# Performance work log

Hardware: AMD Instinct MI355X
Metric: run time of the kernel (lower is better)

## Reference

```python
import jax, jax.numpy as jnp
import numpy as np

B, H, T, D = 2, 16, 2048, 64


def setup_inputs() -> dict:
    key = jax.random.key(0)
    kq, kk, kv, kvm, khm = jax.random.split(key, 5)
    q = jax.random.normal(kq, (B, H, T, D), dtype=jnp.float32)
    k = jax.random.normal(kk, (B, H, D, T), dtype=jnp.float32)  # pre-transposed, matmul(q, k) -> [B,H,T,T]
    v = jax.random.normal(kv, (B, H, T, D), dtype=jnp.float32)
    f = jnp.asarray(float(np.sqrt(D)), dtype=jnp.float32)  # scale divisor
    vmask = (jax.random.uniform(kvm, (B, T)) < 0.9).astype(jnp.float32)
    hmask = (jax.random.uniform(khm, (B, T)) < 0.9).astype(jnp.float32)
    return {"q": q, "k": k, "v": v, "f": f, "vmask": vmask, "hmask": hmask}


def reference(q, k, v, f, vmask, hmask):
    # scores = q @ k / f  -> [B,H,T,T]
    scores = jnp.matmul(q, k) / f
    # padding mask: vmask indexes columns (key positions), hmask indexes rows (query positions)
    pad = vmask[:, None, None, :] * hmask[:, None, :, None]  # [B,1,T,T], broadcasts over H
    s = scores * pad
    s = jnp.where(s == 0, jnp.asarray(1e-10, s.dtype), s)  # masked_fill(new_scores == 0, 1e-10)
    # causal mask: -inf strictly above diagonal
    t = s.shape[-1]
    causal = jnp.triu(jnp.full((t, t), -jnp.inf, dtype=s.dtype), k=1)
    s = s + causal
    return jnp.matmul(jax.nn.softmax(s, axis=-1), v)  # [B,H,T,D]
```

## Files before the change

### kernel.cpp

```cpp
#include <hip/hip_runtime.h>
#include <hip/hip_bf16.h>

#define B_ 2
#define H_ 16
#define T_ 2048
#define D_ 64
#define BH (B_*H_)

typedef __attribute__((ext_vector_type(8))) short bf16x8;
typedef __attribute__((ext_vector_type(16))) float f32x16;
typedef __attribute__((ext_vector_type(4))) unsigned int u32x4;
typedef unsigned int u32;

typedef __attribute__((address_space(3))) void lds_void;
typedef __attribute__((address_space(1))) const void gbl_void;

__device__ __forceinline__ ushort f2bu(float x){
    __hip_bfloat16 h = __float2bfloat16(x);
    return __builtin_bit_cast(ushort, h);
}
__device__ __forceinline__ u32 cvtpk(float a, float b){
    u32 r; asm("v_cvt_pk_bf16_f32 %0, %1, %2" : "=v"(r) : "v"(a), "v"(b)); return r;
}
__device__ __forceinline__ float xhalf_max(float x){
    float a = x, b = x;
    asm("" : "+v"(b));
    asm("v_permlane32_swap_b32 %0, %1" : "+v"(a), "+v"(b));
    return fmaxf(a, b);
}
__device__ __forceinline__ float xhalf_sum(float x){
    float a = x, b = x;
    asm("" : "+v"(b));
    asm("v_permlane32_swap_b32 %0, %1" : "+v"(a), "+v"(b));
    return a + b;
}

__global__ __launch_bounds__(256) void prep(
    const float* __restrict__ k, const float* __restrict__ v,
    const float* __restrict__ vm,
    ushort* __restrict__ KT, ushort* __restrict__ VT)
{
    __shared__ ushort tl[64][65];
    const int bh = blockIdx.x;
    const bool isK = (blockIdx.y < 32);
    const int ty = isK ? blockIdx.y : (blockIdx.y - 32);
    const int i0 = isK ? 0 : ty*64;
    const int j0 = isK ? ty*64 : 0;
    const int M = isK ? D_ : T_;
    const int N = isK ? T_ : D_;
    const float* s = (isK ? k : v) + (size_t)bh*M*N;
    ushort*      d = (isK ? KT : VT) + (size_t)bh*M*N;
    const int tid = threadIdx.x;
    const int rr = tid>>4, c4 = (tid&15)*4;
    #pragma unroll
    for (int p=0;p<4;++p){
        int a = p*16+rr;
        float4 x = *reinterpret_cast<const float4*>(&s[(size_t)(i0+a)*N + j0 + c4]);
        tl[c4+0][a]=f2bu(x.x); tl[c4+1][a]=f2bu(x.y);
        tl[c4+2][a]=f2bu(x.z); tl[c4+3][a]=f2bu(x.w);
    }
    __syncthreads();
    #pragma unroll
    for (int p=0;p<4;++p){
        int bb = p*16+rr;
        ushort4 u;
        u.x=tl[bb][c4]; u.y=tl[bb][c4+1]; u.z=tl[bb][c4+2]; u.w=tl[bb][c4+3];
        if (isK && vm[(size_t)(bh>>4)*T_ + j0 + bb] == 0.f) { u.x=0;u.y=0;u.z=0;u.w=0; }
        *reinterpret_cast<ushort4*>(&d[(size_t)(j0+bb)*M + i0 + c4]) = u;
    }
}

__global__ __launch_bounds__(64, 2) void attn_fwd(
    const float* __restrict__ q, const float* __restrict__ fp,
    const float* __restrict__ hmask,
    const ushort* __restrict__ KT,
    const ushort* __restrict__ VT,
    float* __restrict__ out)
{
    __shared__ __align__(16) ushort sbuf[2][8192];

    const int bid = blockIdx.x;
    const int bh = bid & (BH-1);
    const int qw = 63 - (bid >> 5);
    const int i0 = qw*32;
    const int lane = threadIdx.x & 63;
    const int col = lane & 31;
    const int hi  = lane >> 5;

    const ushort* KTb = KT + (size_t)bh*T_*D_;
    const ushort* VTb = VT + (size_t)bh*T_*D_;

    const float hmv = hmask[(size_t)(bh>>4)*T_ + i0 + col];
    const float sscale = 1.4426950408889634f / fp[0];
    const float qs = (hmv != 0.f) ? sscale : 0.f;
    const float NINF = -__builtin_inff();

    const float* qp = q + (size_t)bh*T_*D_ + (size_t)(i0+col)*D_ + hi*8;
    bf16x8 qf[4];
    #pragma unroll
    for (int dc=0; dc<4; ++dc){
        float4 x0 = *reinterpret_cast<const float4*>(qp + dc*16);
        float4 x1 = *reinterpret_cast<const float4*>(qp + dc*16 + 4);
        u32x4 dw;
        dw[0] = cvtpk(x0.x*qs, x0.y*qs);
        dw[1] = cvtpk(x0.z*qs, x0.w*qs);
        dw[2] = cvtpk(x1.x*qs, x1.y*qs);
        dw[3] = cvtpk(x1.z*qs, x1.w*qs);
        qf[dc] = __builtin_bit_cast(bf16x8, dw);
    }

    float m_run = NINF, l_run = 0.f;
    f32x16 o0, o1;
    #pragma unroll
    for (int r=0;r<16;++r){ o0[r]=0.f; o1[r]=0.f; }

    const unsigned uoff = (unsigned)(lane*16);
    const unsigned swz = ((unsigned)(col&7)) << 4;

    auto stage = [&](int b, int t){
        char* ldsK = (char*)&sbuf[b][0];
        char* ldsV = (char*)&sbuf[b][4096];
        const char* kbase = (const char*)KTb + (size_t)t*8192;
        #pragma unroll
        for (int i=0;i<8;++i){
            const unsigned u = i*1024u + uoff;
            const unsigned su = u ^ (((u>>7)&7u)<<4);
            __builtin_amdgcn_global_load_lds(
                (gbl_void*)(kbase + su),
                (lds_void*)(ldsK + i*1024), 16, 0, 0);
        }
        #pragma unroll
        for (int i=0;i<8;++i){
            const unsigned u = i*1024u + uoff;
            const unsigned dR = u>>7;
            const unsigned inr = (u&127u) ^ ((dR&7u)<<4);
            const char* src = (const char*)VTb + (size_t)dR*(T_*2) + (size_t)t*128 + inr;
            __builtin_amdgcn_global_load_lds(
                (gbl_void*)src,
                (lds_void*)(ldsV + i*1024), 16, 0, 0);
        }
    };

    const int n = (qw >> 1) + 1;
    int buf = 0;
    stage(0, 0);
    asm volatile("s_waitcnt vmcnt(0)" ::: "memory");

    for (int t=0; t<n; ++t){
        const int j0 = t*64;
        if (t+1 < n) stage(buf^1, t+1);

        const char* sKb = (const char*)&sbuf[buf][0];
        bf16x8 kf[8];
        #pragma unroll
        for (int kt=0;kt<2;++kt)
            #pragma unroll
            for (int dc=0;dc<4;++dc)
                kf[kt*4+dc] = *reinterpret_cast<const bf16x8*>(
                    sKb + (((unsigned)(kt*4096 + dc*32 + col*128 + hi*16)) ^ swz));

        f32x16 s0, s1;
        #pragma unroll
        for (int r=0;r<16;++r){ s0[r]=0.f; s1[r]=0.f; }
        #pragma unroll
        for (int dc=0;dc<4;++dc){
            s0 = __builtin_amdgcn_mfma_f32_32x32x16_bf16(kf[dc],   qf[dc], s0, 0,0,0);
            s1 = __builtin_amdgcn_mfma_f32_32x32x16_bf16(kf[4+dc], qf[dc], s1, 0,0,0);
        }

        const char* sVb = (const char*)&sbuf[buf][4096];
        bf16x8 vf[8];
        #pragma unroll
        for (int f=0;f<8;++f)
            vf[f] = *reinterpret_cast<const bf16x8*>(
                sVb + (((unsigned)((f>>2)*4096 + (f&3)*32 + col*128 + hi*16)) ^ swz));

        if (j0 + 63 > i0) {
            const int th0 = i0 + col - j0 - 4*hi;
            const int th1 = th0 - 32;
            #pragma unroll
            for (int r=0;r<16;++r){
                const int basr = (r&3) + 8*(r>>2);
                s0[r] = (basr <= th0) ? s0[r] : NINF;
                s1[r] = (basr <= th1) ? s1[r] : NINF;
            }
        }

        float tm[8];
        #pragma unroll
        for (int i=0;i<8;++i)
            tm[i] = fmaxf(fmaxf(s0[2*i], s0[2*i+1]), fmaxf(s1[2*i], s1[2*i+1]));
        #pragma unroll
        for (int st=4; st>=1; st>>=1)
            #pragma unroll
            for (int i=0;i<st;++i) tm[i] = fmaxf(tm[i], tm[i+st]);
        const float mt = xhalf_max(tm[0]);

        if (__any(!(mt <= m_run + 8.0f))) {
            const float mn = fmaxf(m_run, mt);
            const float fac = __builtin_amdgcn_exp2f(m_run - mn);
            m_run = mn;
            l_run *= fac;
            #pragma unroll
            for (int r=0;r<16;++r){ o0[r]*=fac; o1[r]*=fac; }
        }

        float tsum[8];
        #pragma unroll
        for (int i=0;i<8;++i){
            float p00 = __builtin_amdgcn_exp2f(s0[2*i]   - m_run);
            float p01 = __builtin_amdgcn_exp2f(s0[2*i+1] - m_run);
            float p10 = __builtin_amdgcn_exp2f(s1[2*i]   - m_run);
            float p11 = __builtin_amdgcn_exp2f(s1[2*i+1] - m_run);
            s0[2*i]=p00; s0[2*i+1]=p01; s1[2*i]=p10; s1[2*i+1]=p11;
            tsum[i] = (p00+p01) + (p10+p11);
        }
        #pragma unroll
        for (int st=4; st>=1; st>>=1)
            #pragma unroll
            for (int i=0;i<st;++i) tsum[i] += tsum[i+st];
        l_run += xhalf_sum(tsum[0]);

        bf16x8 pb[4];
        #pragma unroll
        for (int c2=0;c2<4;++c2){
            const f32x16& ps = (c2<2) ? s0 : s1;
            const int rb = (c2&1)*8;
            u32 a0 = cvtpk(ps[rb+0], ps[rb+1]);
            u32 a1 = cvtpk(ps[rb+2], ps[rb+3]);
            u32 a2 = cvtpk(ps[rb+4], ps[rb+5]);
            u32 a3 = cvtpk(ps[rb+6], ps[rb+7]);
            asm("v_permlane32_swap_b32 %0, %1" : "+v"(a0), "+v"(a2));
            asm("v_permlane32_swap_b32 %0, %1" : "+v"(a1), "+v"(a3));
            u32x4 dw; dw[0]=a0; dw[1]=a1; dw[2]=a2; dw[3]=a3;
            pb[c2] = __builtin_bit_cast(bf16x8, dw);
        }

        #pragma unroll
        for (int c2=0;c2<4;++c2){
            o0 = __builtin_amdgcn_mfma_f32_32x32x16_bf16(vf[c2],   pb[c2], o0, 0,0,0);
            o1 = __builtin_amdgcn_mfma_f32_32x32x16_bf16(vf[4+c2], pb[c2], o1, 0,0,0);
        }

        asm volatile("s_waitcnt vmcnt(0)" ::: "memory");
        buf ^= 1;
    }

    const float rinv = 1.0f / l_run;
    float* op = out + (size_t)bh*T_*D_ + (size_t)(i0+col)*D_;
    #pragma unroll
    for (int q4=0;q4<4;++q4){
        float4 a = {o0[4*q4]*rinv, o0[4*q4+1]*rinv, o0[4*q4+2]*rinv, o0[4*q4+3]*rinv};
        *reinterpret_cast<float4*>(op + 8*q4 + 4*hi) = a;
        float4 b = {o1[4*q4]*rinv, o1[4*q4+1]*rinv, o1[4*q4+2]*rinv, o1[4*q4+3]*rinv};
        *reinterpret_cast<float4*>(op + 32 + 8*q4 + 4*hi) = b;
    }
}

extern "C" void kernel_launch(void* const* d_in, const int* in_sizes, int n_in,
                              void* d_out, int out_size, void* d_ws, size_t ws_size,
                              hipStream_t stream) {
    const float* q  = (const float*)d_in[0];
    const float* k  = (const float*)d_in[1];
    const float* v  = (const float*)d_in[2];
    const float* f  = (const float*)d_in[3];
    const float* vm = (const float*)d_in[4];
    const float* hm = (const float*)d_in[5];
    float* out = (float*)d_out;

    const size_t slab = (size_t)BH * T_ * D_;
    ushort* KT = (ushort*)d_ws;
    ushort* VT = KT + slab;

    hipLaunchKernelGGL(prep, dim3(BH, 64), dim3(256), 0, stream, k, v, vm, KT, VT);

    dim3 grid(2048);
    dim3 block(64);
    hipLaunchKernelGGL(attn_fwd, grid, block, 0, stream, q, f, hm, KT, VT, out);
}
```

Baseline: 57.25 us.

## Process two 32-row query tiles per wave to reuse staged K/V tiles

```diff
diff --git a/kernel.cpp b/kernel.cpp
--- a/kernel.cpp
+++ b/kernel.cpp
@@ -81,8 +81,9 @@
 
     const int bid = blockIdx.x;
     const int bh = bid & (BH-1);
-    const int qw = 63 - (bid >> 5);
-    const int i0 = qw*32;
+    const int idx = bid >> 5;
+    const int qw = (bid < 512) ? (31 - idx) : (idx - 16);
+    const int i0 = qw*64;
     const int lane = threadIdx.x & 63;
     const int col = lane & 31;
     const int hi  = lane >> 5;
@@ -90,29 +91,42 @@
     const ushort* KTb = KT + (size_t)bh*T_*D_;
     const ushort* VTb = VT + (size_t)bh*T_*D_;
 
-    const float hmv = hmask[(size_t)(bh>>4)*T_ + i0 + col];
     const float sscale = 1.4426950408889634f / fp[0];
-    const float qs = (hmv != 0.f) ? sscale : 0.f;
+    const float hmA = hmask[(size_t)(bh>>4)*T_ + i0 + col];
+    const float hmB = hmask[(size_t)(bh>>4)*T_ + i0 + 32 + col];
+    const float qsA = (hmA != 0.f) ? sscale : 0.f;
+    const float qsB = (hmB != 0.f) ? sscale : 0.f;
     const float NINF = -__builtin_inff();
 
-    const float* qp = q + (size_t)bh*T_*D_ + (size_t)(i0+col)*D_ + hi*8;
-    bf16x8 qf[4];
+    bf16x8 qfA[4], qfB[4];
+    {
+        const float* qpA = q + (size_t)bh*T_*D_ + (size_t)(i0+col)*D_ + hi*8;
+        const float* qpB = qpA + 32*D_;
+        #pragma unroll
+        for (int dc=0; dc<4; ++dc){
+            float4 x0 = *reinterpret_cast<const float4*>(qpA + dc*16);
+            float4 x1 = *reinterpret_cast<const float4*>(qpA + dc*16 + 4);
+            u32x4 dw;
+            dw[0] = cvtpk(x0.x*qsA, x0.y*qsA);
+            dw[1] = cvtpk(x0.z*qsA, x0.w*qsA);
+            dw[2] = cvtpk(x1.x*qsA, x1.y*qsA);
+            dw[3] = cvtpk(x1.z*qsA, x1.w*qsA);
+            qfA[dc] = __builtin_bit_cast(bf16x8, dw);
+            float4 y0 = *reinterpret_cast<const float4*>(qpB + dc*16);
+            float4 y1 = *reinterpret_cast<const float4*>(qpB + dc*16 + 4);
+            u32x4 ew;
+            ew[0] = cvtpk(y0.x*qsB, y0.y*qsB);
+            ew[1] = cvtpk(y0.z*qsB, y0.w*qsB);
+            ew[2] = cvtpk(y1.x*qsB, y1.y*qsB);
+            ew[3] = cvtpk(y1.z*qsB, y1.w*qsB);
+            qfB[dc] = __builtin_bit_cast(bf16x8, ew);
+        }
+    }
+
+    float mA = 0.f, lA = 0.f, mB = 0.f, lB = 0.f;
+    f32x16 oA0, oA1, oB0, oB1;
     #pragma unroll
-    for (int dc=0; dc<4; ++dc){
-        float4 x0 = *reinterpret_cast<const float4*>(qp + dc*16);
-        float4 x1 = *reinterpret_cast<const float4*>(qp + dc*16 + 4);
-        u32x4 dw;
-        dw[0] = cvtpk(x0.x*qs, x0.y*qs);
-        dw[1] = cvtpk(x0.z*qs, x0.w*qs);
-        dw[2] = cvtpk(x1.x*qs, x1.y*qs);
-        dw[3] = cvtpk(x1.z*qs, x1.w*qs);
-        qf[dc] = __builtin_bit_cast(bf16x8, dw);
-    }
-
-    float m_run = NINF, l_run = 0.f;
-    f32x16 o0, o1;
-    #pragma unroll
-    for (int r=0;r<16;++r){ o0[r]=0.f; o1[r]=0.f; }
+    for (int r=0;r<16;++r){ oA0[r]=0.f; oA1[r]=0.f; oB0[r]=0.f; oB1[r]=0.f; }
 
     const unsigned uoff = (unsigned)(lane*16);
     const unsigned swz = ((unsigned)(col&7)) << 4;
@@ -141,7 +155,7 @@
         }
     };
 
-    const int n = (qw >> 1) + 1;
+    const int n = qw + 1;
     int buf = 0;
     stage(0, 0);
     asm volatile("s_waitcnt vmcnt(0)" ::: "memory");
@@ -159,13 +173,15 @@
                 kf[kt*4+dc] = *reinterpret_cast<const bf16x8*>(
                     sKb + (((unsigned)(kt*4096 + dc*32 + col*128 + hi*16)) ^ swz));
 
-        f32x16 s0, s1;
-        #pragma unroll
-        for (int r=0;r<16;++r){ s0[r]=0.f; s1[r]=0.f; }
+        f32x16 sA0, sA1, sB0, sB1;
+        #pragma unroll
+        for (int r=0;r<16;++r){ sA0[r]=0.f; sA1[r]=0.f; sB0[r]=0.f; sB1[r]=0.f; }
         #pragma unroll
         for (int dc=0;dc<4;++dc){
-            s0 = __builtin_amdgcn_mfma_f32_32x32x16_bf16(kf[dc],   qf[dc], s0, 0,0,0);
-            s1 = __builtin_amdgcn_mfma_f32_32x32x16_bf16(kf[4+dc], qf[dc], s1, 0,0,0);
+            sA0 = __builtin_amdgcn_mfma_f32_32x32x16_bf16(kf[dc],   qfA[dc], sA0, 0,0,0);
+            sA1 = __builtin_amdgcn_mfma_f32_32x32x16_bf16(kf[4+dc], qfA[dc], sA1, 0,0,0);
+            sB0 = __builtin_amdgcn_mfma_f32_32x32x16_bf16(kf[dc],   qfB[dc], sB0, 0,0,0);
+            sB1 = __builtin_amdgcn_mfma_f32_32x32x16_bf16(kf[4+dc], qfB[dc], sB1, 0,0,0);
         }
 
         const char* sVb = (const char*)&sbuf[buf][4096];
@@ -176,84 +192,146 @@
                 sVb + (((unsigned)((f>>2)*4096 + (f&3)*32 + col*128 + hi*16)) ^ swz));
 
         if (j0 + 63 > i0) {
-            const int th0 = i0 + col - j0 - 4*hi;
-            const int th1 = th0 - 32;
+            const int thA0 = i0 + col - j0 - 4*hi,      thA1 = thA0 - 32;
+            const int thB0 = i0 + 32 + col - j0 - 4*hi, thB1 = thB0 - 32;
             #pragma unroll
             for (int r=0;r<16;++r){
                 const int basr = (r&3) + 8*(r>>2);
-                s0[r] = (basr <= th0) ? s0[r] : NINF;
-                s1[r] = (basr <= th1) ? s1[r] : NINF;
-            }
-        }
-
-        float tm[8];
-        #pragma unroll
-        for (int i=0;i<8;++i)
-            tm[i] = fmaxf(fmaxf(s0[2*i], s0[2*i+1]), fmaxf(s1[2*i], s1[2*i+1]));
-        #pragma unroll
-        for (int st=4; st>=1; st>>=1)
-            #pragma unroll
-            for (int i=0;i<st;++i) tm[i] = fmaxf(tm[i], tm[i+st]);
-        const float mt = xhalf_max(tm[0]);
-
-        if (__any(!(mt <= m_run + 8.0f))) {
-            const float mn = fmaxf(m_run, mt);
-            const float fac = __builtin_amdgcn_exp2f(m_run - mn);
-            m_run = mn;
-            l_run *= fac;
-            #pragma unroll
-            for (int r=0;r<16;++r){ o0[r]*=fac; o1[r]*=fac; }
-        }
-
-        float tsum[8];
-        #pragma unroll
-        for (int i=0;i<8;++i){
-            float p00 = __builtin_amdgcn_exp2f(s0[2*i]   - m_run);
-            float p01 = __builtin_amdgcn_exp2f(s0[2*i+1] - m_run);
-            float p10 = __builtin_amdgcn_exp2f(s1[2*i]   - m_run);
-            float p11 = __builtin_amdgcn_exp2f(s1[2*i+1] - m_run);
-            s0[2*i]=p00; s0[2*i+1]=p01; s1[2*i]=p10; s1[2*i+1]=p11;
-            tsum[i] = (p00+p01) + (p10+p11);
-        }
-        #pragma unroll
-        for (int st=4; st>=1; st>>=1)
-            #pragma unroll
-            for (int i=0;i<st;++i) tsum[i] += tsum[i+st];
-        l_run += xhalf_sum(tsum[0]);
-
-        bf16x8 pb[4];
-        #pragma unroll
-        for (int c2=0;c2<4;++c2){
-            const f32x16& ps = (c2<2) ? s0 : s1;
-            const int rb = (c2&1)*8;
-            u32 a0 = cvtpk(ps[rb+0], ps[rb+1]);
-            u32 a1 = cvtpk(ps[rb+2], ps[rb+3]);
-            u32 a2 = cvtpk(ps[rb+4], ps[rb+5]);
-            u32 a3 = cvtpk(ps[rb+6], ps[rb+7]);
-            asm("v_permlane32_swap_b32 %0, %1" : "+v"(a0), "+v"(a2));
-            asm("v_permlane32_swap_b32 %0, %1" : "+v"(a1), "+v"(a3));
-            u32x4 dw; dw[0]=a0; dw[1]=a1; dw[2]=a2; dw[3]=a3;
-            pb[c2] = __builtin_bit_cast(bf16x8, dw);
-        }
-
-        #pragma unroll
-        for (int c2=0;c2<4;++c2){
-            o0 = __builtin_amdgcn_mfma_f32_32x32x16_bf16(vf[c2],   pb[c2], o0, 0,0,0);
-            o1 = __builtin_amdgcn_mfma_f32_32x32x16_bf16(vf[4+c2], pb[c2], o1, 0,0,0);
+                sA0[r] = (basr <= thA0) ? sA0[r] : NINF;
+                sA1[r] = (basr <= thA1) ? sA1[r] : NINF;
+                sB0[r] = (basr <= thB0) ? sB0[r] : NINF;
+                sB1[r] = (basr <= thB1) ? sB1[r] : NINF;
+            }
+        }
+
+        {
+            float tm[8];
+            #pragma unroll
+            for (int i=0;i<8;++i)
+                tm[i] = fmaxf(fmaxf(sA0[2*i], sA0[2*i+1]), fmaxf(sA1[2*i], sA1[2*i+1]));
+            #pragma unroll
+            for (int st=4; st>=1; st>>=1)
+                #pragma unroll
+                for (int i=0;i<st;++i) tm[i] = fmaxf(tm[i], tm[i+st]);
+            const float mt = xhalf_max(tm[0]);
+            if (__any(!(mt <= mA + 8.0f))) {
+                const float mn = fmaxf(mA, mt);
+                const float fac = __builtin_amdgcn_exp2f(mA - mn);
+                mA = mn; lA *= fac;
+                #pragma unroll
+                for (int r=0;r<16;++r){ oA0[r]*=fac; oA1[r]*=fac; }
+            }
+            float tsum[8];
+            #pragma unroll
+            for (int i=0;i<8;++i){
+                float p00 = __builtin_amdgcn_exp2f(sA0[2*i]   - mA);
+                float p01 = __builtin_amdgcn_exp2f(sA0[2*i+1] - mA);
+                float p10 = __builtin_amdgcn_exp2f(sA1[2*i]   - mA);
+                float p11 = __builtin_amdgcn_exp2f(sA1[2*i+1] - mA);
+                sA0[2*i]=p00; sA0[2*i+1]=p01; sA1[2*i]=p10; sA1[2*i+1]=p11;
+                tsum[i] = (p00+p01) + (p10+p11);
+            }
+            #pragma unroll
+            for (int st=4; st>=1; st>>=1)
+                #pragma unroll
+                for (int i=0;i<st;++i) tsum[i] += tsum[i+st];
+            lA += xhalf_sum(tsum[0]);
+
+            bf16x8 pb[4];
+            #pragma unroll
+            for (int c2=0;c2<4;++c2){
+                const f32x16& ps = (c2<2) ? sA0 : sA1;
+                const int rb = (c2&1)*8;
+                u32 a0 = cvtpk(ps[rb+0], ps[rb+1]);
+                u32 a1 = cvtpk(ps[rb+2], ps[rb+3]);
+                u32 a2 = cvtpk(ps[rb+4], ps[rb+5]);
+                u32 a3 = cvtpk(ps[rb+6], ps[rb+7]);
+                asm("v_permlane32_swap_b32 %0, %1" : "+v"(a0), "+v"(a2));
+                asm("v_permlane32_swap_b32 %0, %1" : "+v"(a1), "+v"(a3));
+                u32x4 dw; dw[0]=a0; dw[1]=a1; dw[2]=a2; dw[3]=a3;
+                pb[c2] = __builtin_bit_cast(bf16x8, dw);
+            }
+            #pragma unroll
+            for (int c2=0;c2<4;++c2){
+                oA0 = __builtin_amdgcn_mfma_f32_32x32x16_bf16(vf[c2],   pb[c2], oA0, 0,0,0);
+                oA1 = __builtin_amdgcn_mfma_f32_32x32x16_bf16(vf[4+c2], pb[c2], oA1, 0,0,0);
+            }
+        }
+
+        {
+            float tm[8];
+            #pragma unroll
+            for (int i=0;i<8;++i)
+                tm[i] = fmaxf(fmaxf(sB0[2*i], sB0[2*i+1]), fmaxf(sB1[2*i], sB1[2*i+1]));
+            #pragma unroll
+            for (int st=4; st>=1; st>>=1)
+                #pragma unroll
+                for (int i=0;i<st;++i) tm[i] = fmaxf(tm[i], tm[i+st]);
+            const float mt = xhalf_max(tm[0]);
+            if (__any(!(mt <= mB + 8.0f))) {
+                const float mn = fmaxf(mB, mt);
+                const float fac = __builtin_amdgcn_exp2f(mB - mn);
+                mB = mn; lB *= fac;
+                #pragma unroll
+                for (int r=0;r<16;++r){ oB0[r]*=fac; oB1[r]*=fac; }
+            }
+            float tsum[8];
+            #pragma unroll
+            for (int i=0;i<8;++i){
+                float p00 = __builtin_amdgcn_exp2f(sB0[2*i]   - mB);
+                float p01 = __builtin_amdgcn_exp2f(sB0[2*i+1] - mB);
+                float p10 = __builtin_amdgcn_exp2f(sB1[2*i]   - mB);
+                float p11 = __builtin_amdgcn_exp2f(sB1[2*i+1] - mB);
+                sB0[2*i]=p00; sB0[2*i+1]=p01; sB1[2*i]=p10; sB1[2*i+1]=p11;
+                tsum[i] = (p00+p01) + (p10+p11);
+            }
+            #pragma unroll
+            for (int st=4; st>=1; st>>=1)
+                #pragma unroll
+                for (int i=0;i<st;++i) tsum[i] += tsum[i+st];
+            lB += xhalf_sum(tsum[0]);
+
+            bf16x8 pb[4];
+            #pragma unroll
+            for (int c2=0;c2<4;++c2){
+                const f32x16& ps = (c2<2) ? sB0 : sB1;
+                const int rb = (c2&1)*8;
+                u32 a0 = cvtpk(ps[rb+0], ps[rb+1]);
+                u32 a1 = cvtpk(ps[rb+2], ps[rb+3]);
+                u32 a2 = cvtpk(ps[rb+4], ps[rb+5]);
+                u32 a3 = cvtpk(ps[rb+6], ps[rb+7]);
+                asm("v_permlane32_swap_b32 %0, %1" : "+v"(a0), "+v"(a2));
+                asm("v_permlane32_swap_b32 %0, %1" : "+v"(a1), "+v"(a3));
+                u32x4 dw; dw[0]=a0; dw[1]=a1; dw[2]=a2; dw[3]=a3;
+                pb[c2] = __builtin_bit_cast(bf16x8, dw);
+            }
+            #pragma unroll
+            for (int c2=0;c2<4;++c2){
+                oB0 = __builtin_amdgcn_mfma_f32_32x32x16_bf16(vf[c2],   pb[c2], oB0, 0,0,0);
+                oB1 = __builtin_amdgcn_mfma_f32_32x32x16_bf16(vf[4+c2], pb[c2], oB1, 0,0,0);
+            }
         }
 
         asm volatile("s_waitcnt vmcnt(0)" ::: "memory");
         buf ^= 1;
     }
 
-    const float rinv = 1.0f / l_run;
-    float* op = out + (size_t)bh*T_*D_ + (size_t)(i0+col)*D_;
-    #pragma unroll
-    for (int q4=0;q4<4;++q4){
-        float4 a = {o0[4*q4]*rinv, o0[4*q4+1]*rinv, o0[4*q4+2]*rinv, o0[4*q4+3]*rinv};
-        *reinterpret_cast<float4*>(op + 8*q4 + 4*hi) = a;
-        float4 b = {o1[4*q4]*rinv, o1[4*q4+1]*rinv, o1[4*q4+2]*rinv, o1[4*q4+3]*rinv};
-        *reinterpret_cast<float4*>(op + 32 + 8*q4 + 4*hi) = b;
+    {
+        const float riA = 1.0f / lA;
+        float* opA = out + (size_t)bh*T_*D_ + (size_t)(i0+col)*D_;
+        const float riB = 1.0f / lB;
+        float* opB = opA + 32*D_;
+        #pragma unroll
+        for (int q4=0;q4<4;++q4){
+            float4 a = {oA0[4*q4]*riA, oA0[4*q4+1]*riA, oA0[4*q4+2]*riA, oA0[4*q4+3]*riA};
+            *reinterpret_cast<float4*>(opA + 8*q4 + 4*hi) = a;
+            float4 b = {oA1[4*q4]*riA, oA1[4*q4+1]*riA, oA1[4*q4+2]*riA, oA1[4*q4+3]*riA};
+            *reinterpret_cast<float4*>(opA + 32 + 8*q4 + 4*hi) = b;
+            float4 c = {oB0[4*q4]*riB, oB0[4*q4+1]*riB, oB0[4*q4+2]*riB, oB0[4*q4+3]*riB};
+            *reinterpret_cast<float4*>(opB + 8*q4 + 4*hi) = c;
+            float4 d = {oB1[4*q4]*riB, oB1[4*q4+1]*riB, oB1[4*q4+2]*riB, oB1[4*q4+3]*riB};
+            *reinterpret_cast<float4*>(opB + 32 + 8*q4 + 4*hi) = d;
+        }
     }
 }
 
@@ -274,7 +352,7 @@
 
     hipLaunchKernelGGL(prep, dim3(BH, 64), dim3(256), 0, stream, k, v, vm, KT, VT);
 
-    dim3 grid(2048);
+    dim3 grid(1024);
     dim3 block(64);
     hipLaunchKernelGGL(attn_fwd, grid, block, 0, stream, q, f, hm, KT, VT, out);
 }
```

New measurement: 66.08 us. 15.4% more time.

## Share K/V tiles across four waves per block and pair causal query blocks

Applied to the files above, without the earlier changes.

```diff
diff --git a/kernel.cpp b/kernel.cpp
--- a/kernel.cpp
+++ b/kernel.cpp
@@ -70,7 +70,7 @@
     }
 }
 
-__global__ __launch_bounds__(64, 2) void attn_fwd(
+__global__ __launch_bounds__(256, 2) void attn_fwd(
     const float* __restrict__ q, const float* __restrict__ fp,
     const float* __restrict__ hmask,
     const ushort* __restrict__ KT,
@@ -81,40 +81,19 @@
 
     const int bid = blockIdx.x;
     const int bh = bid & (BH-1);
-    const int qw = 63 - (bid >> 5);
-    const int i0 = qw*32;
-    const int lane = threadIdx.x & 63;
+    const int pr = bid >> 5;
+    const int tid = threadIdx.x;
+    const int lane = tid & 63;
+    const int wid  = tid >> 6;
     const int col = lane & 31;
     const int hi  = lane >> 5;
 
     const ushort* KTb = KT + (size_t)bh*T_*D_;
     const ushort* VTb = VT + (size_t)bh*T_*D_;
-
-    const float hmv = hmask[(size_t)(bh>>4)*T_ + i0 + col];
     const float sscale = 1.4426950408889634f / fp[0];
-    const float qs = (hmv != 0.f) ? sscale : 0.f;
     const float NINF = -__builtin_inff();
 
-    const float* qp = q + (size_t)bh*T_*D_ + (size_t)(i0+col)*D_ + hi*8;
-    bf16x8 qf[4];
-    #pragma unroll
-    for (int dc=0; dc<4; ++dc){
-        float4 x0 = *reinterpret_cast<const float4*>(qp + dc*16);
-        float4 x1 = *reinterpret_cast<const float4*>(qp + dc*16 + 4);
-        u32x4 dw;
-        dw[0] = cvtpk(x0.x*qs, x0.y*qs);
-        dw[1] = cvtpk(x0.z*qs, x0.w*qs);
-        dw[2] = cvtpk(x1.x*qs, x1.y*qs);
-        dw[3] = cvtpk(x1.z*qs, x1.w*qs);
-        qf[dc] = __builtin_bit_cast(bf16x8, dw);
-    }
-
-    float m_run = NINF, l_run = 0.f;
-    f32x16 o0, o1;
-    #pragma unroll
-    for (int r=0;r<16;++r){ o0[r]=0.f; o1[r]=0.f; }
-
-    const unsigned uoff = (unsigned)(lane*16);
+    const unsigned uoff = (unsigned)(wid*1024 + lane*16);
     const unsigned swz = ((unsigned)(col&7)) << 4;
 
     auto stage = [&](int b, int t){
@@ -122,138 +101,167 @@
         char* ldsV = (char*)&sbuf[b][4096];
         const char* kbase = (const char*)KTb + (size_t)t*8192;
         #pragma unroll
-        for (int i=0;i<8;++i){
-            const unsigned u = i*1024u + uoff;
+        for (int i=0;i<2;++i){
+            const unsigned u = i*4096u + uoff;
             const unsigned su = u ^ (((u>>7)&7u)<<4);
             __builtin_amdgcn_global_load_lds(
                 (gbl_void*)(kbase + su),
-                (lds_void*)(ldsK + i*1024), 16, 0, 0);
-        }
-        #pragma unroll
-        for (int i=0;i<8;++i){
-            const unsigned u = i*1024u + uoff;
+                (lds_void*)(ldsK + i*4096 + wid*1024), 16, 0, 0);
+        }
+        #pragma unroll
+        for (int i=0;i<2;++i){
+            const unsigned u = i*4096u + uoff;
             const unsigned dR = u>>7;
             const unsigned inr = (u&127u) ^ ((dR&7u)<<4);
             const char* src = (const char*)VTb + (size_t)dR*(T_*2) + (size_t)t*128 + inr;
             __builtin_amdgcn_global_load_lds(
                 (gbl_void*)src,
-                (lds_void*)(ldsV + i*1024), 16, 0, 0);
+                (lds_void*)(ldsV + i*4096 + wid*1024), 16, 0, 0);
         }
     };
 
-    const int n = (qw >> 1) + 1;
-    int buf = 0;
-    stage(0, 0);
-    asm volatile("s_waitcnt vmcnt(0)" ::: "memory");
-
-    for (int t=0; t<n; ++t){
-        const int j0 = t*64;
-        if (t+1 < n) stage(buf^1, t+1);
-
-        const char* sKb = (const char*)&sbuf[buf][0];
-        bf16x8 kf[8];
-        #pragma unroll
-        for (int kt=0;kt<2;++kt)
+    #pragma unroll 1
+    for (int pp=0; pp<2; ++pp){
+        const int qb = pp ? pr : (15 - pr);
+        const int i0w = qb*128 + wid*32;
+
+        const float hmv = hmask[(size_t)(bh>>4)*T_ + i0w + col];
+        const float qs = (hmv != 0.f) ? sscale : 0.f;
+
+        bf16x8 qf[4];
+        {
+            const float* qp = q + (size_t)bh*T_*D_ + (size_t)(i0w+col)*D_ + hi*8;
             #pragma unroll
-            for (int dc=0;dc<4;++dc)
-                kf[kt*4+dc] = *reinterpret_cast<const bf16x8*>(
-                    sKb + (((unsigned)(kt*4096 + dc*32 + col*128 + hi*16)) ^ swz));
-
-        f32x16 s0, s1;
-        #pragma unroll
-        for (int r=0;r<16;++r){ s0[r]=0.f; s1[r]=0.f; }
-        #pragma unroll
-        for (int dc=0;dc<4;++dc){
-            s0 = __builtin_amdgcn_mfma_f32_32x32x16_bf16(kf[dc],   qf[dc], s0, 0,0,0);
-            s1 = __builtin_amdgcn_mfma_f32_32x32x16_bf16(kf[4+dc], qf[dc], s1, 0,0,0);
-        }
-
-        const char* sVb = (const char*)&sbuf[buf][4096];
-        bf16x8 vf[8];
-        #pragma unroll
-        for (int f=0;f<8;++f)
-            vf[f] = *reinterpret_cast<const bf16x8*>(
-                sVb + (((unsigned)((f>>2)*4096 + (f&3)*32 + col*128 + hi*16)) ^ swz));
-
-        if (j0 + 63 > i0) {
-            const int th0 = i0 + col - j0 - 4*hi;
-            const int th1 = th0 - 32;
-            #pragma unroll
-            for (int r=0;r<16;++r){
-                const int basr = (r&3) + 8*(r>>2);
-                s0[r] = (basr <= th0) ? s0[r] : NINF;
-                s1[r] = (basr <= th1) ? s1[r] : NINF;
+            for (int dc=0; dc<4; ++dc){
+                float4 x0 = *reinterpret_cast<const float4*>(qp + dc*16);
+                float4 x1 = *reinterpret_cast<const float4*>(qp + dc*16 + 4);
+                u32x4 dw;
+                dw[0] = cvtpk(x0.x*qs, x0.y*qs);
+                dw[1] = cvtpk(x0.z*qs, x0.w*qs);
+                dw[2] = cvtpk(x1.x*qs, x1.y*qs);
+                dw[3] = cvtpk(x1.z*qs, x1.w*qs);
+                qf[dc] = __builtin_bit_cast(bf16x8, dw);
             }
         }
 
-        float tm[8];
-        #pragma unroll
-        for (int i=0;i<8;++i)
-            tm[i] = fmaxf(fmaxf(s0[2*i], s0[2*i+1]), fmaxf(s1[2*i], s1[2*i+1]));
-        #pragma unroll
-        for (int st=4; st>=1; st>>=1)
-            #pragma unroll
-            for (int i=0;i<st;++i) tm[i] = fmaxf(tm[i], tm[i+st]);
-        const float mt = xhalf_max(tm[0]);
-
-        if (__any(!(mt <= m_run + 8.0f))) {
-            const float mn = fmaxf(m_run, mt);
-            const float fac = __builtin_amdgcn_exp2f(m_run - mn);
-            m_run = mn;
-            l_run *= fac;
-            #pragma unroll
-            for (int r=0;r<16;++r){ o0[r]*=fac; o1[r]*=fac; }
-        }
-
-        float tsum[8];
-        #pragma unroll
-        for (int i=0;i<8;++i){
-            float p00 = __builtin_amdgcn_exp2f(s0[2*i]   - m_run);
-            float p01 = __builtin_amdgcn_exp2f(s0[2*i+1] - m_run);
-            float p10 = __builtin_amdgcn_exp2f(s1[2*i]   - m_run);
-            float p11 = __builtin_amdgcn_exp2f(s1[2*i+1] - m_run);
-            s0[2*i]=p00; s0[2*i+1]=p01; s1[2*i]=p10; s1[2*i+1]=p11;
-            tsum[i] = (p00+p01) + (p10+p11);
-        }
-        #pragma unroll
-        for (int st=4; st>=1; st>>=1)
-            #pragma unroll
-            for (int i=0;i<st;++i) tsum[i] += tsum[i+st];
-        l_run += xhalf_sum(tsum[0]);
-
-        bf16x8 pb[4];
-        #pragma unroll
-        for (int c2=0;c2<4;++c2){
-            const f32x16& ps = (c2<2) ? s0 : s1;
-            const int rb = (c2&1)*8;
-            u32 a0 = cvtpk(ps[rb+0], ps[rb+1]);
-            u32 a1 = cvtpk(ps[rb+2], ps[rb+3]);
-            u32 a2 = cvtpk(ps[rb+4], ps[rb+5]);
-            u32 a3 = cvtpk(ps[rb+6], ps[rb+7]);
-            asm("v_permlane32_swap_b32 %0, %1" : "+v"(a0), "+v"(a2));
-            asm("v_permlane32_swap_b32 %0, %1" : "+v"(a1), "+v"(a3));
-            u32x4 dw; dw[0]=a0; dw[1]=a1; dw[2]=a2; dw[3]=a3;
-            pb[c2] = __builtin_bit_cast(bf16x8, dw);
-        }
-
-        #pragma unroll
-        for (int c2=0;c2<4;++c2){
-            o0 = __builtin_amdgcn_mfma_f32_32x32x16_bf16(vf[c2],   pb[c2], o0, 0,0,0);
-            o1 = __builtin_amdgcn_mfma_f32_32x32x16_bf16(vf[4+c2], pb[c2], o1, 0,0,0);
-        }
-
-        asm volatile("s_waitcnt vmcnt(0)" ::: "memory");
-        buf ^= 1;
-    }
-
-    const float rinv = 1.0f / l_run;
-    float* op = out + (size_t)bh*T_*D_ + (size_t)(i0+col)*D_;
-    #pragma unroll
-    for (int q4=0;q4<4;++q4){
-        float4 a = {o0[4*q4]*rinv, o0[4*q4+1]*rinv, o0[4*q4+2]*rinv, o0[4*q4+3]*rinv};
-        *reinterpret_cast<float4*>(op + 8*q4 + 4*hi) = a;
-        float4 b = {o1[4*q4]*rinv, o1[4*q4+1]*rinv, o1[4*q4+2]*rinv, o1[4*q4+3]*rinv};
-        *reinterpret_cast<float4*>(op + 32 + 8*q4 + 4*hi) = b;
+        float m_run = 0.f, l_run = 0.f;
+        f32x16 o0, o1;
+        #pragma unroll
+        for (int r=0;r<16;++r){ o0[r]=0.f; o1[r]=0.f; }
+
+        const int n = 2*qb + 2;
+        int bsel = 0;
+        __syncthreads();
+        stage(0, 0);
+
+        for (int it=0; it<n; ++it){
+            const int j0 = it*64;
+            __syncthreads();
+            if (it+1 < n) stage(bsel^1, it+1);
+
+            if (j0 <= i0w + 31){
+                const char* sKb = (const char*)&sbuf[bsel][0];
+                bf16x8 kf[8];
+                #pragma unroll
+                for (int kt=0;kt<2;++kt)
+                    #pragma unroll
+                    for (int dc=0;dc<4;++dc)
+                        kf[kt*4+dc] = *reinterpret_cast<const bf16x8*>(
+                            sKb + (((unsigned)(kt*4096 + dc*32 + col*128 + hi*16)) ^ swz));
+
+                f32x16 s0, s1;
+                #pragma unroll
+                for (int r=0;r<16;++r){ s0[r]=0.f; s1[r]=0.f; }
+                #pragma unroll
+                for (int dc=0;dc<4;++dc){
+                    s0 = __builtin_amdgcn_mfma_f32_32x32x16_bf16(kf[dc],   qf[dc], s0, 0,0,0);
+                    s1 = __builtin_amdgcn_mfma_f32_32x32x16_bf16(kf[4+dc], qf[dc], s1, 0,0,0);
+                }
+
+                const char* sVb = (const char*)&sbuf[bsel][4096];
+                bf16x8 vf[8];
+                #pragma unroll
+                for (int f=0;f<8;++f)
+                    vf[f] = *reinterpret_cast<const bf16x8*>(
+                        sVb + (((unsigned)((f>>2)*4096 + (f&3)*32 + col*128 + hi*16)) ^ swz));
+
+                if (j0 + 63 > i0w) {
+                    const int th0 = i0w + col - j0 - 4*hi;
+                    const int th1 = th0 - 32;
+                    #pragma unroll
+                    for (int r=0;r<16;++r){
+                        const int basr = (r&3) + 8*(r>>2);
+                        s0[r] = (basr <= th0) ? s0[r] : NINF;
+                        s1[r] = (basr <= th1) ? s1[r] : NINF;
+                    }
+                }
+
+                float tm[8];
+                #pragma unroll
+                for (int i=0;i<8;++i)
+                    tm[i] = fmaxf(fmaxf(s0[2*i], s0[2*i+1]), fmaxf(s1[2*i], s1[2*i+1]));
+                #pragma unroll
+                for (int st=4; st>=1; st>>=1)
+                    #pragma unroll
+                    for (int i=0;i<st;++i) tm[i] = fmaxf(tm[i], tm[i+st]);
+                const float mt = xhalf_max(tm[0]);
+                if (__any(!(mt <= m_run + 8.0f))) {
+                    const float mn = fmaxf(m_run, mt);
+                    const float fac = __builtin_amdgcn_exp2f(m_run - mn);
+                    m_run = mn; l_run *= fac;
+                    #pragma unroll
+                    for (int r=0;r<16;++r){ o0[r]*=fac; o1[r]*=fac; }
+                }
+
+                float tsum[8];
+                #pragma unroll
+                for (int i=0;i<8;++i){
+                    float p00 = __builtin_amdgcn_exp2f(s0[2*i]   - m_run);
+                    float p01 = __builtin_amdgcn_exp2f(s0[2*i+1] - m_run);
+                    float p10 = __builtin_amdgcn_exp2f(s1[2*i]   - m_run);
+                    float p11 = __builtin_amdgcn_exp2f(s1[2*i+1] - m_run);
+                    s0[2*i]=p00; s0[2*i+1]=p01; s1[2*i]=p10; s1[2*i+1]=p11;
+                    tsum[i] = (p00+p01) + (p10+p11);
+                }
+                #pragma unroll
+                for (int st=4; st>=1; st>>=1)
+                    #pragma unroll
+                    for (int i=0;i<st;++i) tsum[i] += tsum[i+st];
+                l_run += xhalf_sum(tsum[0]);
+
+                bf16x8 pb[4];
+                #pragma unroll
+                for (int c2=0;c2<4;++c2){
+                    const f32x16& ps = (c2<2) ? s0 : s1;
+                    const int rb = (c2&1)*8;
+                    u32 a0 = cvtpk(ps[rb+0], ps[rb+1]);
+                    u32 a1 = cvtpk(ps[rb+2], ps[rb+3]);
+                    u32 a2 = cvtpk(ps[rb+4], ps[rb+5]);
+                    u32 a3 = cvtpk(ps[rb+6], ps[rb+7]);
+                    asm("v_permlane32_swap_b32 %0, %1" : "+v"(a0), "+v"(a2));
+                    asm("v_permlane32_swap_b32 %0, %1" : "+v"(a1), "+v"(a3));
+                    u32x4 dw; dw[0]=a0; dw[1]=a1; dw[2]=a2; dw[3]=a3;
+                    pb[c2] = __builtin_bit_cast(bf16x8, dw);
+                }
+
+                #pragma unroll
+                for (int c2=0;c2<4;++c2){
+                    o0 = __builtin_amdgcn_mfma_f32_32x32x16_bf16(vf[c2],   pb[c2], o0, 0,0,0);
+                    o1 = __builtin_amdgcn_mfma_f32_32x32x16_bf16(vf[4+c2], pb[c2], o1, 0,0,0);
+                }
+            }
+            bsel ^= 1;
+        }
+
+        const float rinv = 1.0f / l_run;
+        float* op = out + (size_t)bh*T_*D_ + (size_t)(i0w+col)*D_;
+        #pragma unroll
+        for (int q4=0;q4<4;++q4){
+            float4 a = {o0[4*q4]*rinv, o0[4*q4+1]*rinv, o0[4*q4+2]*rinv, o0[4*q4+3]*rinv};
+            *reinterpret_cast<float4*>(op + 8*q4 + 4*hi) = a;
+            float4 b = {o1[4*q4]*rinv, o1[4*q4+1]*rinv, o1[4*q4+2]*rinv, o1[4*q4+3]*rinv};
+            *reinterpret_cast<float4*>(op + 32 + 8*q4 + 4*hi) = b;
+        }
     }
 }
 
@@ -274,7 +282,7 @@
 
     hipLaunchKernelGGL(prep, dim3(BH, 64), dim3(256), 0, stream, k, v, vm, KT, VT);
 
-    dim3 grid(2048);
-    dim3 block(64);
+    dim3 grid(256);
+    dim3 block(256);
     hipLaunchKernelGGL(attn_fwd, grid, block, 0, stream, q, f, hm, KT, VT, out);
 }
```

Result: faster. 53.74 us (-6.1%).
